# Kernel tuning notes

Hardware: AMD Instinct MI355X
Metric: run time of the kernel (lower is better)

Reference implementation:

```python
import jax, jax.numpy as jnp
import numpy as np

DELTA = 1
DROP_DC = False
EPS = 1e-8


def _shell_labels(D, H, W, delta):
    # radial frequency magnitude in cycles/voxel, assuming cubic-ish volume
    fx = jnp.fft.fftfreq(D)[:, None, None]
    fy = jnp.fft.fftfreq(H)[None, :, None]
    fz = jnp.fft.fftfreq(W)[None, None, :]
    r = jnp.sqrt(fx * fx + fy * fy + fz * fz)  # [D,H,W]
    n = min(D, H, W)
    nbins = n // (2 * delta)          # shells up to Nyquist (0.5 cyc/voxel)
    df = delta / n                    # shell width in frequency units
    labels = jnp.minimum((r / df).astype(jnp.int32), nbins)  # overflow bin = nbins
    return labels.reshape(-1), nbins


def setup_inputs() -> dict:
    key = jax.random.key(0)
    k1, k2 = jax.random.split(key)
    shape = (2, 1, 256, 256, 256)
    img_ref = jax.random.normal(k1, shape, dtype=jnp.float32)
    img_pred = jax.random.normal(k2, shape, dtype=jnp.float32)
    return {"img_ref": img_ref, "img_pred": img_pred}


def reference(img_ref, img_pred):
    B, C, D, H, W = img_ref.shape
    labels, nbins = _shell_labels(D, H, W, DELTA)

    F1 = jnp.fft.fftn(img_ref, axes=(-3, -2, -1))   # complex64 [B,C,D,H,W]
    F2 = jnp.fft.fftn(img_pred, axes=(-3, -2, -1))

    cross = jnp.real(F1 * jnp.conj(F2)).reshape(B * C, -1)
    p1 = (jnp.real(F1) ** 2 + jnp.imag(F1) ** 2).reshape(B * C, -1)
    p2 = (jnp.real(F2) ** 2 + jnp.imag(F2) ** 2).reshape(B * C, -1)

    def seg(x):  # radial shell sum; drop the overflow bin beyond Nyquist
        return jax.ops.segment_sum(x, labels, num_segments=nbins + 1)[:nbins]

    num = jax.vmap(seg)(cross)   # [B*C, nbins]
    d1 = jax.vmap(seg)(p1)
    d2 = jax.vmap(seg)(p2)

    fsc = num / jnp.sqrt(d1 * d2 + EPS)
    if DROP_DC:
        fsc = fsc[:, 1:]
    loss = 1.0 - jnp.mean(fsc ** 2)
    return loss
```

## Files before the change

kernel.cpp:

```cpp
#include <hip/hip_runtime.h>
#include <math.h>

#define NDIM 256
#define VOL  (NDIM*NDIM*NDIM)
#define NB   128

__device__ __forceinline__ int dr4(int x) {
    int b = (int)(__brev((unsigned)x) >> 24);
    return ((b >> 1) & 0x55) | ((b << 1) & 0xAA);
}
__device__ __forceinline__ float2 cmul(float2 a, float2 b) {
    return make_float2(a.x * b.x - a.y * b.y, a.x * b.y + a.y * b.x);
}
__device__ __forceinline__ float2 cadd(float2 a, float2 b){ return make_float2(a.x+b.x, a.y+b.y); }
__device__ __forceinline__ float2 csub(float2 a, float2 b){ return make_float2(a.x-b.x, a.y-b.y); }
__device__ __forceinline__ float2 cmuli_neg(float2 a){ return make_float2(a.y, -a.x); }
__device__ __forceinline__ float2 cmuli_pos(float2 a){ return make_float2(-a.y, a.x); }

__global__ __launch_bounds__(256) void fftz_pack(const float* __restrict__ re_in,
                                                 const float* __restrict__ im_in,
                                                 float2* __restrict__ out)
{
    __shared__ float2 buf[4][2][NDIM];
    const int t = threadIdx.x;
    const int w = t >> 6, j = t & 63;
    const int L = blockIdx.x * 4 + w;
    const float* rp = re_in + (size_t)L * NDIM;
    const float* ip = im_in + (size_t)L * NDIM;

    float2 v0 = make_float2(rp[j      ], ip[j      ]);
    float2 v1 = make_float2(rp[j +  64], ip[j +  64]);
    float2 v2 = make_float2(rp[j + 128], ip[j + 128]);
    float2 v3 = make_float2(rp[j + 192], ip[j + 192]);

    {
        float2 t0=cadd(v0,v2), t1=csub(v0,v2), t2=cadd(v1,v3), t3=csub(v1,v3);
        buf[w][0][4*j    ] = cadd(t0, t2);
        buf[w][0][4*j + 1] = cadd(t1, cmuli_neg(t3));
        buf[w][0][4*j + 2] = csub(t0, t2);
        buf[w][0][4*j + 3] = cadd(t1, cmuli_pos(t3));
    }
    __builtin_amdgcn_sched_barrier(0);

    int p = 0;
    #pragma unroll
    for (int stage = 1; stage <= 2; ++stage) {
        const int Ns = (stage == 1) ? 4 : 16;
        const int jm = j & (Ns - 1);
        float2 a0 = buf[w][p][j      ];
        float2 a1 = buf[w][p][j +  64];
        float2 a2 = buf[w][p][j + 128];
        float2 a3 = buf[w][p][j + 192];
        float sn, cs;
        __sincosf(-(float)(2.0 * M_PI) * (float)jm / (float)(4 * Ns), &sn, &cs);
        float2 w1 = make_float2(cs, sn);
        float2 w2 = cmul(w1, w1);
        float2 w3 = cmul(w2, w1);
        a1 = cmul(a1, w1); a2 = cmul(a2, w2); a3 = cmul(a3, w3);
        float2 t0=cadd(a0,a2), t1=csub(a0,a2), t2=cadd(a1,a3), t3=csub(a1,a3);
        const int idxD = (j / Ns) * (4 * Ns) + jm;
        buf[w][p^1][idxD         ] = cadd(t0, t2);
        buf[w][p^1][idxD +     Ns] = cadd(t1, cmuli_neg(t3));
        buf[w][p^1][idxD + 2 * Ns] = csub(t0, t2);
        buf[w][p^1][idxD + 3 * Ns] = cadd(t1, cmuli_pos(t3));
        p ^= 1;
        __builtin_amdgcn_sched_barrier(0);
    }

    {
        float2 a0 = buf[w][p][j      ];
        float2 a1 = buf[w][p][j +  64];
        float2 a2 = buf[w][p][j + 128];
        float2 a3 = buf[w][p][j + 192];
        float sn, cs;
        __sincosf(-(float)(2.0 * M_PI) * (float)j / 256.0f, &sn, &cs);
        float2 w1 = make_float2(cs, sn);
        float2 w2 = cmul(w1, w1);
        float2 w3 = cmul(w2, w1);
        a1 = cmul(a1, w1); a2 = cmul(a2, w2); a3 = cmul(a3, w3);
        float2 t0=cadd(a0,a2), t1=csub(a0,a2), t2=cadd(a1,a3), t3=csub(a1,a3);
        float2* op = out + (size_t)L * NDIM;
        op[j      ] = cadd(t0, t2);
        op[j +  64] = cadd(t1, cmuli_neg(t3));
        op[j + 128] = csub(t0, t2);
        op[j + 192] = cadd(t1, cmuli_pos(t3));
    }
}

__global__ __launch_bounds__(256) void fft_strided(float2* __restrict__ A,
                                                   int lineStride, int outerStride)
{
    __shared__ float2 tile[NDIM * 18];
    __shared__ float2 tw[NDIM];
    const int t = threadIdx.x;
    {
        float sn, cs;
        __sincosf(-(float)(2.0 * M_PI) * (float)t / 256.0f, &sn, &cs);
        tw[t] = make_float2(cs, sn);
    }
    const int l4 = t & 7, u8 = t >> 3;
    const int o = blockIdx.x >> 4, c = blockIdx.x & 15;
    const long long base = (long long)o * outerStride + c * 16;

    #pragma unroll
    for (int it = 0; it < 8; ++it) {
        int pos = u8 + it * 32;
        const float4 d = *(const float4*)&A[base + (long long)pos * lineStride + 2 * l4];
        tile[pos * 18 + 2 * l4    ] = make_float2(d.x, d.y);
        tile[pos * 18 + 2 * l4 + 1] = make_float2(d.z, d.w);
    }
    __syncthreads();

    const int l = t & 15, u = t >> 4;
    #pragma unroll
    for (int ls = 6; ls >= 0; ls -= 2) {
        const int s = 1 << ls;
        #pragma unroll
        for (int it = 0; it < 4; ++it) {
            int m  = u + it * 16;
            int jm = m & (s - 1);
            int bidx = ((m >> ls) << (ls + 2)) + jm;
            float2 a  = tile[(bidx        ) * 18 + l];
            float2 b  = tile[(bidx +     s) * 18 + l];
            float2 cc = tile[(bidx + 2 * s) * 18 + l];
            float2 d  = tile[(bidx + 3 * s) * 18 + l];
            float2 t0=cadd(a,cc), t1=csub(a,cc), t2=cadd(b,d), t3=csub(b,d);
            float2 y0 = cadd(t0, t2);
            float2 y1 = cadd(t1, cmuli_neg(t3));
            float2 y2 = csub(t0, t2);
            float2 y3 = cadd(t1, cmuli_pos(t3));
            int k1 = jm << (6 - ls);
            y1 = cmul(y1, tw[k1]);
            y2 = cmul(y2, tw[2 * k1]);
            y3 = cmul(y3, tw[3 * k1]);
            tile[(bidx        ) * 18 + l] = y0;
            tile[(bidx +     s) * 18 + l] = y1;
            tile[(bidx + 2 * s) * 18 + l] = y2;
            tile[(bidx + 3 * s) * 18 + l] = y3;
        }
        __syncthreads();
    }

    #pragma unroll
    for (int it = 0; it < 8; ++it) {
        int pos = u8 + it * 32;
        float2 e0 = tile[pos * 18 + 2 * l4], e1 = tile[pos * 18 + 2 * l4 + 1];
        *(float4*)&A[base + (long long)pos * lineStride + 2 * l4] =
            make_float4(e0.x, e0.y, e1.x, e1.y);
    }
}

__global__ __launch_bounds__(256) void reduce_shells(const float2* __restrict__ A,
                                                     float* __restrict__ bins)
{
    __shared__ float bs[4][3 * NB];
    const int t = threadIdx.x;
    const int w = t >> 6;
    for (int i = t; i < 4 * 3 * NB; i += 256) ((float*)bs)[i] = 0.f;
    __syncthreads();

    const int pz  = t;
    const int izc = (pz < 128) ? pz : 256 - pz;
    const int iz2 = izc * izc;
    const int pzp = (256 - pz) & 255;

    float2 z1[8], z2[8];
    int   lc2[8];
    float wgt[8];

    #pragma unroll
    for (int jj = 0; jj < 8; ++jj) {
        int L = blockIdx.x * 8 + jj;
        int px = L >> 8, py = L & 255;
        int fx = dr4(px), fy = dr4(py);
        int fxp = (256 - fx) & 255, fyp = (256 - fy) & 255;
        int Lp = dr4(fxp) * 256 + dr4(fyp);
        int ax = (fx < 128) ? fx : 256 - fx;
        int ay = (fy < 128) ? fy : 256 - fy;
        int c2 = ax * ax + ay * ay;
        lc2[jj] = -1;
        if (Lp < L) continue;
        if (c2 >= NB * NB) continue;
        lc2[jj] = c2;
        wgt[jj] = (Lp == L) ? 1.f : 2.f;
        z1[jj] = A[(long long)L  * 256 + pz];
        z2[jj] = A[(long long)Lp * 256 + pzp];
    }

    #pragma unroll
    for (int jj = 0; jj < 8; ++jj) {
        if (lc2[jj] < 0) continue;
        int m = lc2[jj] + iz2;
        int lab = (int)sqrtf((float)m);
        if (lab >= NB) continue;
        float2 a = z1[jj], b = z2[jj];
        float F1r = 0.5f * (a.x + b.x);
        float F1i = 0.5f * (a.y - b.y);
        float F2r = 0.5f * (a.y + b.y);
        float F2i = 0.5f * (b.x - a.x);
        float g = wgt[jj];
        atomicAdd(&bs[w][lab],           g * (F1r * F2r + F1i * F2i));
        atomicAdd(&bs[w][NB + lab],      g * (F1r * F1r + F1i * F1i));
        atomicAdd(&bs[w][2 * NB + lab],  g * (F2r * F2r + F2i * F2i));
    }
    __syncthreads();
    for (int i = t; i < 3 * NB; i += 256) {
        float v = bs[0][i] + bs[1][i] + bs[2][i] + bs[3][i];
        if (v != 0.f) atomicAdd(&bins[i], v);
    }
}

__global__ void zero_bins(float* bins)
{
    int t = blockIdx.x * blockDim.x + threadIdx.x;
    if (t < 2 * 3 * NB) bins[t] = 0.f;
}

__global__ void finalize(const float* __restrict__ binsAll, float* __restrict__ out)
{
    __shared__ float red[256];
    const int t = threadIdx.x;
    const int b = t >> 7, bin = t & 127;
    const float* bb = binsAll + b * 3 * NB;
    float num = bb[bin], d1 = bb[NB + bin], d2 = bb[2 * NB + bin];
    float fsc = num / sqrtf(d1 * d2 + 1e-8f);
    red[t] = fsc * fsc;
    __syncthreads();
    for (int s = 128; s > 0; s >>= 1) {
        if (t < s) red[t] += red[t + s];
        __syncthreads();
    }
    if (t == 0) out[0] = 1.f - red[0] / 256.f;
}

__global__ void ws_too_small(float* out) { out[0] = -1.0e9f; }

extern "C" void kernel_launch(void* const* d_in, const int* in_sizes, int n_in,
                              void* d_out, int out_size, void* d_ws, size_t ws_size,
                              hipStream_t stream)
{
    const float* ref  = (const float*)d_in[0];
    const float* pred = (const float*)d_in[1];
    float* out = (float*)d_out;

    const size_t volBytes = (size_t)VOL * sizeof(float2);
    if (ws_size < volBytes + 4096) {
        ws_too_small<<<1, 1, 0, stream>>>(out);
        return;
    }
    float2* A   = (float2*)d_ws;
    float* bins = (float*)((char*)d_ws + volBytes);

    zero_bins<<<1, 1024, 0, stream>>>(bins);

    for (int b = 0; b < 2; ++b) {
        fftz_pack  <<<16384, 256, 0, stream>>>(ref + (size_t)b * VOL,
                                               pred + (size_t)b * VOL, A);
        fft_strided<<<4096, 256, 0, stream>>>(A, 256,   65536);
        fft_strided<<<4096, 256, 0, stream>>>(A, 65536, 256);
        reduce_shells<<<8192, 256, 0, stream>>>(A, bins + b * 3 * NB);
    }
    finalize<<<1, 256, 0, stream>>>(bins, out);
}
```

Before: 668.3 us.

## Fuse final x-axis FFT with radial shell reduction and spread bin atomics

Removes the last strided FFT pass and the separate reduction kernel by doing the x-axis FFT in shared memory for a y-plane and a 16-column chunk, together with its conjugate-mirror partner tile. It then accumulates the shell sums directly from shared memory, which saves a full write and read of the volume. It only loads the half-space of columns that is needed (2048 blocks), and spreads the global bin atomics over 16 copies that finalize sums. The cost is larger shared-memory use per block and more complex indexing.

```diff
diff --git a/kernel.cpp b/kernel.cpp
--- a/kernel.cpp
+++ b/kernel.cpp
@@ -4,6 +4,7 @@
 #define NDIM 256
 #define VOL  (NDIM*NDIM*NDIM)
 #define NB   128
+#define NSPREAD 16
 
 __device__ __forceinline__ int dr4(int x) {
     int b = (int)(__brev((unsigned)x) >> 24);
@@ -150,79 +151,139 @@
     }
 }
 
-__global__ __launch_bounds__(256) void reduce_shells(const float2* __restrict__ A,
-                                                     float* __restrict__ bins)
-{
-    __shared__ float bs[4][3 * NB];
+__global__ __launch_bounds__(256) void fft_x_reduce(const float2* __restrict__ A,
+                                                    float* __restrict__ bins_s)
+{
+    __shared__ float2 tA[NDIM * 17];
+    __shared__ float2 tB[NDIM * 17];
+    __shared__ float2 tw[NDIM];
+    __shared__ float  bs[4][3 * NB];
     const int t = threadIdx.x;
     const int w = t >> 6;
+    const int fy = blockIdx.x >> 4, c = blockIdx.x & 15;
+    const int py  = dr4(fy);
+    const int pyp = dr4((256 - fy) & 255);
+    const float wgt = (fy == 0) ? 1.f : 2.f;
+    const int ay2 = fy * fy;
+
+    {
+        float sn, cs;
+        __sincosf(-(float)(2.0 * M_PI) * (float)t / 256.0f, &sn, &cs);
+        tw[t] = make_float2(cs, sn);
+    }
     for (int i = t; i < 4 * 3 * NB; i += 256) ((float*)bs)[i] = 0.f;
+
+    {
+        const int zi = t & 15, u = t >> 4;
+        const int z = (16 * c + 1 + zi) & 255;
+        const long long off = (long long)py * 256 + z;
+        #pragma unroll
+        for (int it = 0; it < 16; ++it) {
+            int pos = u + it * 16;
+            tA[pos * 17 + zi] = A[(long long)pos * 65536 + off];
+        }
+    }
+    {
+        const int l4 = t & 7, u8 = t >> 3;
+        const long long off = (long long)pyp * 256 + (240 - 16 * c);
+        #pragma unroll
+        for (int it = 0; it < 8; ++it) {
+            int pos = u8 + it * 32;
+            const float4 d = *(const float4*)&A[(long long)pos * 65536 + off + 2 * l4];
+            tB[pos * 17 + 2 * l4    ] = make_float2(d.x, d.y);
+            tB[pos * 17 + 2 * l4 + 1] = make_float2(d.z, d.w);
+        }
+    }
     __syncthreads();
 
-    const int pz  = t;
-    const int izc = (pz < 128) ? pz : 256 - pz;
-    const int iz2 = izc * izc;
-    const int pzp = (256 - pz) & 255;
-
-    float2 z1[8], z2[8];
-    int   lc2[8];
-    float wgt[8];
-
-    #pragma unroll
-    for (int jj = 0; jj < 8; ++jj) {
-        int L = blockIdx.x * 8 + jj;
-        int px = L >> 8, py = L & 255;
-        int fx = dr4(px), fy = dr4(py);
-        int fxp = (256 - fx) & 255, fyp = (256 - fy) & 255;
-        int Lp = dr4(fxp) * 256 + dr4(fyp);
-        int ax = (fx < 128) ? fx : 256 - fx;
-        int ay = (fy < 128) ? fy : 256 - fy;
-        int c2 = ax * ax + ay * ay;
-        lc2[jj] = -1;
-        if (Lp < L) continue;
-        if (c2 >= NB * NB) continue;
-        lc2[jj] = c2;
-        wgt[jj] = (Lp == L) ? 1.f : 2.f;
-        z1[jj] = A[(long long)L  * 256 + pz];
-        z2[jj] = A[(long long)Lp * 256 + pzp];
-    }
-
-    #pragma unroll
-    for (int jj = 0; jj < 8; ++jj) {
-        if (lc2[jj] < 0) continue;
-        int m = lc2[jj] + iz2;
-        int lab = (int)sqrtf((float)m);
-        if (lab >= NB) continue;
-        float2 a = z1[jj], b = z2[jj];
-        float F1r = 0.5f * (a.x + b.x);
-        float F1i = 0.5f * (a.y - b.y);
-        float F2r = 0.5f * (a.y + b.y);
-        float F2i = 0.5f * (b.x - a.x);
-        float g = wgt[jj];
-        atomicAdd(&bs[w][lab],           g * (F1r * F2r + F1i * F2i));
-        atomicAdd(&bs[w][NB + lab],      g * (F1r * F1r + F1i * F1i));
-        atomicAdd(&bs[w][2 * NB + lab],  g * (F2r * F2r + F2i * F2i));
+    const int l = t & 15, u = t >> 4;
+    #pragma unroll
+    for (int ls = 6; ls >= 0; ls -= 2) {
+        const int s = 1 << ls;
+        #pragma unroll
+        for (int half = 0; half < 2; ++half) {
+            float2* tile = half ? tB : tA;
+            #pragma unroll
+            for (int it = 0; it < 4; ++it) {
+                int m  = u + it * 16;
+                int jm = m & (s - 1);
+                int bidx = ((m >> ls) << (ls + 2)) + jm;
+                float2 a  = tile[(bidx        ) * 17 + l];
+                float2 b  = tile[(bidx +     s) * 17 + l];
+                float2 cc = tile[(bidx + 2 * s) * 17 + l];
+                float2 d  = tile[(bidx + 3 * s) * 17 + l];
+                float2 t0=cadd(a,cc), t1=csub(a,cc), t2=cadd(b,d), t3=csub(b,d);
+                float2 y0 = cadd(t0, t2);
+                float2 y1 = cadd(t1, cmuli_neg(t3));
+                float2 y2 = csub(t0, t2);
+                float2 y3 = cadd(t1, cmuli_pos(t3));
+                int k1 = jm << (6 - ls);
+                y1 = cmul(y1, tw[k1]);
+                y2 = cmul(y2, tw[2 * k1]);
+                y3 = cmul(y3, tw[3 * k1]);
+                tile[(bidx        ) * 17 + l] = y0;
+                tile[(bidx +     s) * 17 + l] = y1;
+                tile[(bidx + 2 * s) * 17 + l] = y2;
+                tile[(bidx + 3 * s) * 17 + l] = y3;
+            }
+        }
+        __syncthreads();
+    }
+
+    {
+        const int zi = l;
+        const int z  = (16 * c + 1 + zi) & 255;
+        const int az = (z < 128) ? z : 256 - z;
+        const int r2yz = az * az + ay2;
+        const int colp = 15 - zi;
+        #pragma unroll
+        for (int it = 0; it < 16; ++it) {
+            int pos = u + it * 16;
+            int fx = dr4(pos);
+            int ax = (fx < 128) ? fx : 256 - fx;
+            int m = ax * ax + r2yz;
+            if (m >= NB * NB) continue;
+            int lab = (int)sqrtf((float)m);
+            int posp = dr4((256 - fx) & 255);
+            float2 a = tA[pos * 17 + zi];
+            float2 b = tB[posp * 17 + colp];
+            float F1r = 0.5f * (a.x + b.x);
+            float F1i = 0.5f * (a.y - b.y);
+            float F2r = 0.5f * (a.y + b.y);
+            float F2i = 0.5f * (b.x - a.x);
+            atomicAdd(&bs[w][lab],          wgt * (F1r * F2r + F1i * F2i));
+            atomicAdd(&bs[w][NB + lab],     wgt * (F1r * F1r + F1i * F1i));
+            atomicAdd(&bs[w][2 * NB + lab], wgt * (F2r * F2r + F2i * F2i));
+        }
     }
     __syncthreads();
+
+    float* dst = bins_s + (blockIdx.x & (NSPREAD - 1)) * (3 * NB);
     for (int i = t; i < 3 * NB; i += 256) {
         float v = bs[0][i] + bs[1][i] + bs[2][i] + bs[3][i];
-        if (v != 0.f) atomicAdd(&bins[i], v);
+        if (v != 0.f) atomicAdd(&dst[i], v);
     }
 }
 
 __global__ void zero_bins(float* bins)
 {
     int t = blockIdx.x * blockDim.x + threadIdx.x;
-    if (t < 2 * 3 * NB) bins[t] = 0.f;
-}
-
-__global__ void finalize(const float* __restrict__ binsAll, float* __restrict__ out)
+    if (t < 2 * NSPREAD * 3 * NB) bins[t] = 0.f;
+}
+
+__global__ void finalize(const float* __restrict__ bins_s, float* __restrict__ out)
 {
     __shared__ float red[256];
     const int t = threadIdx.x;
     const int b = t >> 7, bin = t & 127;
-    const float* bb = binsAll + b * 3 * NB;
-    float num = bb[bin], d1 = bb[NB + bin], d2 = bb[2 * NB + bin];
+    const float* base = bins_s + (size_t)b * NSPREAD * 3 * NB;
+    float num = 0.f, d1 = 0.f, d2 = 0.f;
+    #pragma unroll
+    for (int s = 0; s < NSPREAD; ++s) {
+        num += base[s * 3 * NB + bin];
+        d1  += base[s * 3 * NB + NB + bin];
+        d2  += base[s * 3 * NB + 2 * NB + bin];
+    }
     float fsc = num / sqrtf(d1 * d2 + 1e-8f);
     red[t] = fsc * fsc;
     __syncthreads();
@@ -244,21 +305,21 @@
     float* out = (float*)d_out;
 
     const size_t volBytes = (size_t)VOL * sizeof(float2);
-    if (ws_size < volBytes + 4096) {
+    const size_t binBytes = (size_t)2 * NSPREAD * 3 * NB * sizeof(float);
+    if (ws_size < volBytes + binBytes) {
         ws_too_small<<<1, 1, 0, stream>>>(out);
         return;
     }
-    float2* A   = (float2*)d_ws;
-    float* bins = (float*)((char*)d_ws + volBytes);
-
-    zero_bins<<<1, 1024, 0, stream>>>(bins);
+    float2* A     = (float2*)d_ws;
+    float* bins_s = (float*)((char*)d_ws + volBytes);
+
+    zero_bins<<<(2 * NSPREAD * 3 * NB + 1023) / 1024, 1024, 0, stream>>>(bins_s);
 
     for (int b = 0; b < 2; ++b) {
-        fftz_pack  <<<16384, 256, 0, stream>>>(ref + (size_t)b * VOL,
-                                               pred + (size_t)b * VOL, A);
-        fft_strided<<<4096, 256, 0, stream>>>(A, 256,   65536);
-        fft_strided<<<4096, 256, 0, stream>>>(A, 65536, 256);
-        reduce_shells<<<8192, 256, 0, stream>>>(A, bins + b * 3 * NB);
-    }
-    finalize<<<1, 256, 0, stream>>>(bins, out);
-}
+        fftz_pack   <<<16384, 256, 0, stream>>>(ref + (size_t)b * VOL,
+                                                pred + (size_t)b * VOL, A);
+        fft_strided <<<4096, 256, 0, stream>>>(A, 256, 65536);
+        fft_x_reduce<<<2048, 256, 0, stream>>>(A, bins_s + (size_t)b * NSPREAD * 3 * NB);
+    }
+    finalize<<<1, 256, 0, stream>>>(bins_s, out);
+}
```

Result: slower. 711.8 us (+6.5%).
